# Kernel tuning notes

Measured on AMD Instinct MI355X. Metric: run time of the kernel, lower is better.

## Reference

```python
import jax, jax.numpy as jnp
import numpy as np

HSP, WSP = 8, 32
HEADS = 6
EPS = 1e-5


def _ln(x, g, b):
    m = x.mean(-1, keepdims=True)
    v = ((x - m) ** 2).mean(-1, keepdims=True)
    return (x - m) / jnp.sqrt(v + EPS) * g + b


def _pos_mlp(rpe, pw0, pb0, g1, be1, w1, b1, g2, be2, w2, b2, g3, be3, w3, b3):
    # DynamicPosBias (residual=False): pos3(pos2(pos1(pos_proj(biases))))
    x = rpe @ pw0.T + pb0
    x = jax.nn.relu(_ln(x, g1, be1)) @ w1.T + b1
    x = jax.nn.relu(_ln(x, g2, be2)) @ w2.T + b2
    x = jax.nn.relu(_ln(x, g3, be3)) @ w3.T + b3
    return x  # (n_bias, HEADS)


def setup_inputs() -> dict:
    key = jax.random.key(0)
    ks = jax.random.split(key, 8)
    B, H, W, C = 4, 128, 256, 192
    L = H * W
    pd = (C // 4) // 4  # pos_dim = 12
    nbias = (2 * HSP - 1) * (2 * WSP - 1)  # 945
    N = HSP * WSP  # 256
    nW = L // N  # 128
    f32 = jnp.float32
    return {
        "qkv": jax.random.normal(ks[0], (3, B, L, C), f32),
        "mask": jax.random.normal(ks[1], (nW, N, N), f32),
        "rpe_biases": jax.random.normal(ks[2], (nbias, 2), f32),
        "pw0": jax.random.normal(ks[3], (pd, 2), f32) * 0.02,
        "pb0": jnp.zeros((pd,), f32),
        "g1": jnp.ones((pd,), f32),
        "be1": jnp.zeros((pd,), f32),
        "w1": jax.random.normal(ks[4], (pd, pd), f32) * 0.02,
        "b1": jnp.zeros((pd,), f32),
        "g2": jnp.ones((pd,), f32),
        "be2": jnp.zeros((pd,), f32),
        "w2": jax.random.normal(ks[5], (pd, pd), f32) * 0.02,
        "b2": jnp.zeros((pd,), f32),
        "g3": jnp.ones((pd,), f32),
        "be3": jnp.zeros((pd,), f32),
        "w3": jax.random.normal(ks[6], (HEADS, pd), f32) * 0.02,
        "b3": jnp.zeros((HEADS,), f32),
        "rpi": jax.random.randint(ks[7], (N, N), 0, nbias),
        "H": H,
        "W": W,
    }


def reference(qkv, mask, rpe_biases, pw0, pb0, g1, be1, w1, b1, g2, be2, w2, b2, g3, be3, w3, b3, rpi, H, W):
    _, B, L, C = qkv.shape
    hd = C // HEADS
    scale = hd ** -0.5
    N = HSP * WSP

    def im2win(x):  # (B,L,C) -> (B*nW, HEADS, N, hd)
        x = x.reshape(B, H // HSP, HSP, W // WSP, WSP, C)
        x = x.transpose(0, 1, 3, 2, 4, 5).reshape(-1, N, HEADS, hd)
        return x.transpose(0, 2, 1, 3)

    q = im2win(qkv[0]) * scale
    k = im2win(qkv[1])
    v = im2win(qkv[2])
    attn = jnp.einsum('whnd,whmd->whnm', q, k)  # (B*nW, HEADS, N, N)
    pos = _pos_mlp(rpe_biases, pw0, pb0, g1, be1, w1, b1, g2, be2, w2, b2, g3, be3, w3, b3)
    rpb = pos[rpi.reshape(-1)].reshape(N, N, HEADS).transpose(2, 0, 1)  # (HEADS,N,N)
    attn = attn + rpb[None]
    nW = mask.shape[0]
    attn = attn.reshape(B, nW, HEADS, N, N) + mask[None, :, None]
    attn = jax.nn.softmax(attn, axis=-1).reshape(-1, HEADS, N, N)
    x = (attn @ v).transpose(0, 2, 1, 3).reshape(-1, N, C)  # (B*nW, N, C)
    # windows2img
    x = x.reshape(B, H // HSP, W // WSP, HSP, WSP, C).transpose(0, 1, 3, 2, 4, 5).reshape(B, H, W, C)
    return x
```

## Files before the change

### kernel.cpp

```cpp
#include <hip/hip_runtime.h>

#define EPS 1e-5f
#define LOG2E 1.4426950408889634f
#define QSCALE (0.17677669529663687f * 1.4426950408889634f)

typedef __attribute__((ext_vector_type(8))) short bf16x8;
typedef __attribute__((ext_vector_type(4))) float f32x4;

#if __has_builtin(__builtin_amdgcn_exp2f)
#define EXP2F(x) __builtin_amdgcn_exp2f(x)
#else
#define EXP2F(x) exp2f(x)
#endif

__device__ __forceinline__ unsigned short f2bf(float f) {
  unsigned u = __float_as_uint(f);
  return (unsigned short)((u + 0x7FFFu + ((u >> 16) & 1u)) >> 16);
}
__device__ __forceinline__ float bflo(unsigned u) { return __uint_as_float(u << 16); }
__device__ __forceinline__ float bfhi(unsigned u) { return __uint_as_float(u & 0xFFFF0000u); }

__global__ void pos_mlp_kernel(const float* __restrict__ rpe,
                               const float* __restrict__ pw0, const float* __restrict__ pb0,
                               const float* __restrict__ g1, const float* __restrict__ be1,
                               const float* __restrict__ w1, const float* __restrict__ b1,
                               const float* __restrict__ g2, const float* __restrict__ be2,
                               const float* __restrict__ w2, const float* __restrict__ b2,
                               const float* __restrict__ g3, const float* __restrict__ be3,
                               const float* __restrict__ w3, const float* __restrict__ b3,
                               float* __restrict__ posT) {
  int r = blockIdx.x * blockDim.x + threadIdx.x;
  if (r >= 945) return;
  float a = rpe[2 * r], c = rpe[2 * r + 1];
  float x[12], y[12];
#pragma unroll
  for (int i = 0; i < 12; ++i) x[i] = pw0[2 * i] * a + pw0[2 * i + 1] * c + pb0[i];

  auto stage = [&](const float* g, const float* be, const float* w, const float* bb,
                   const float* in, float* outv, int dout) {
    float m = 0.f;
#pragma unroll
    for (int i = 0; i < 12; ++i) m += in[i];
    m *= (1.f / 12.f);
    float v = 0.f;
#pragma unroll
    for (int i = 0; i < 12; ++i) { float d = in[i] - m; v += d * d; }
    v *= (1.f / 12.f);
    float rs = rsqrtf(v + EPS);
    float t[12];
#pragma unroll
    for (int i = 0; i < 12; ++i) t[i] = fmaxf((in[i] - m) * rs * g[i] + be[i], 0.f);
    for (int o = 0; o < dout; ++o) {
      float s = bb[o];
#pragma unroll
      for (int i = 0; i < 12; ++i) s += w[o * 12 + i] * t[i];
      outv[o] = s;
    }
  };
  stage(g1, be1, w1, b1, x, y, 12);
  stage(g2, be2, w2, b2, y, x, 12);
  stage(g3, be3, w3, b3, x, y, 6);
#pragma unroll
  for (int h = 0; h < 6; ++h) posT[h * 945 + r] = y[h];
}

__global__ void rpb_gather_swz(const int* __restrict__ rpi, const float* __restrict__ posT,
                               unsigned short* __restrict__ rpb) {
  int n2 = blockIdx.x * 256 + threadIdx.x;
  int q = n2 >> 8, key = n2 & 255;
  int idx = rpi[n2];
  int s = ((key >> 5) << 13) + (q << 5) + (key & 31);
#pragma unroll
  for (int h = 0; h < 6; ++h) rpb[(h << 16) + s] = f2bf(posT[h * 945 + idx] * LOG2E);
}

__global__ void mask_cvt_swz(const float* __restrict__ src, uint4* __restrict__ dst) {
  int g = blockIdx.x * 256 + threadIdx.x;
  int wimg = g >> 13;
  int rem = g & 8191;
  int q = rem >> 5;
  int k8 = rem & 31;
  const float* m = src + ((size_t)wimg << 16) + (q << 8) + (k8 << 3);
  float4 a0 = *(const float4*)m;
  float4 a1 = *(const float4*)(m + 4);
  unsigned v0 = (unsigned)f2bf(a0.x * LOG2E) | ((unsigned)f2bf(a0.y * LOG2E) << 16);
  unsigned v1 = (unsigned)f2bf(a0.z * LOG2E) | ((unsigned)f2bf(a0.w * LOG2E) << 16);
  unsigned v2 = (unsigned)f2bf(a1.x * LOG2E) | ((unsigned)f2bf(a1.y * LOG2E) << 16);
  unsigned v3 = (unsigned)f2bf(a1.z * LOG2E) | ((unsigned)f2bf(a1.w * LOG2E) << 16);
  uint4 o; o.x = v0; o.y = v1; o.z = v2; o.w = v3;
  dst[(((size_t)wimg << 16) + ((k8 >> 2) << 13) + (q << 5) + ((k8 & 3) << 3)) >> 3] = o;
}

template <int USEBF>
__global__ __launch_bounds__(512, 6) void attn_kernel(
    const float* __restrict__ qkv, const float* __restrict__ maskf,
    const unsigned short* __restrict__ maskb, const unsigned short* __restrict__ rpb,
    float* __restrict__ out) {
  __shared__ unsigned short Kb[10240];
  __shared__ unsigned short Vt[8448];

  const int tid = threadIdx.x;
  const int wv = tid >> 6;
  const int lane = tid & 63;
  const int quad = lane >> 4;
  const int l16 = lane & 15;
  const int wIdx = blockIdx.x, h = blockIdx.y;
  const int b = wIdx >> 7, wimg = wIdx & 127;
  const int wh = wimg >> 3, ww = wimg & 7;

  {
    const int tok = tid >> 3;
    const int c4 = (tid & 7) << 2;
#pragma unroll
    for (int p = 0; p < 4; ++p) {
      int n = (p << 6) + tok;
      int i = n >> 5, j = n & 31;
      int l = ((wh << 3) + i) * 256 + (ww << 5) + j;
      const float* kp = qkv + ((size_t)((4 + b) * 32768 + l)) * 192 + h * 32 + c4;
      const float* vp = qkv + ((size_t)((8 + b) * 32768 + l)) * 192 + h * 32 + c4;
      float4 kk = *(const float4*)kp;
      float4 vvv = *(const float4*)vp;
      unsigned long long pk = (unsigned long long)f2bf(kk.x) |
                              ((unsigned long long)f2bf(kk.y) << 16) |
                              ((unsigned long long)f2bf(kk.z) << 32) |
                              ((unsigned long long)f2bf(kk.w) << 48);
      int c = n & 31;
      int rowp = (n & ~31) | ((c & 4) << 2) | ((c & 24) >> 1) | (c & 3);
      *(unsigned long long*)(&Kb[rowp * 40 + c4]) = pk;
      Vt[(c4 + 0) * 264 + n] = f2bf(vvv.x);
      Vt[(c4 + 1) * 264 + n] = f2bf(vvv.y);
      Vt[(c4 + 2) * 264 + n] = f2bf(vvv.z);
      Vt[(c4 + 3) * 264 + n] = f2bf(vvv.w);
    }
  }

  bf16x8 qf[2];
#pragma unroll
  for (int rt = 0; rt < 2; ++rt) {
    int n = (wv << 5) + (rt << 4) + l16;
    int i = n >> 5, j = n & 31;
    int l = ((wh << 3) + i) * 256 + (ww << 5) + j;
    const float* qp = qkv + ((size_t)(b * 32768 + l)) * 192 + h * 32 + (quad << 3);
    float4 a0 = *(const float4*)qp;
    float4 a1 = *(const float4*)(qp + 4);
    bf16x8 f;
    f[0] = (short)f2bf(a0.x * QSCALE); f[1] = (short)f2bf(a0.y * QSCALE);
    f[2] = (short)f2bf(a0.z * QSCALE); f[3] = (short)f2bf(a0.w * QSCALE);
    f[4] = (short)f2bf(a1.x * QSCALE); f[5] = (short)f2bf(a1.y * QSCALE);
    f[6] = (short)f2bf(a1.z * QSCALE); f[7] = (short)f2bf(a1.w * QSCALE);
    qf[rt] = f;
  }

  __syncthreads();

  f32x4 Oacc[2][2];
#pragma unroll
  for (int rt = 0; rt < 2; ++rt) {
    Oacc[rt][0] = (f32x4){0.f, 0.f, 0.f, 0.f};
    Oacc[rt][1] = (f32x4){0.f, 0.f, 0.f, 0.f};
  }
  float lsum[2] = {0.f, 0.f};

  const unsigned short* rp = rpb + ((size_t)h << 16);
  const unsigned short* mp = maskb + ((size_t)wimg << 16);
  const float* mfp0 = maskf + ((size_t)wimg << 16);
  const int boff = (((wv << 5) + l16) << 5) + (quad << 3);
  const f32x4 zero = (f32x4){0.f, 0.f, 0.f, 0.f};

  for (int cc = 0; cc < 8; ++cc) {
    const int cb = cc << 5;
    const int tof = cc << 13;
    uint4 pr[2], mr[2];
#pragma unroll
    for (int rt = 0; rt < 2; ++rt) {
      int o0 = tof + boff + (rt << 9);
      pr[rt] = *(const uint4*)(rp + o0);
      if (USEBF) mr[rt] = *(const uint4*)(mp + o0);
    }
    bf16x8 kf0 = *(const bf16x8*)(&Kb[(cb + l16) * 40 + (quad << 3)]);
    bf16x8 kf1 = *(const bf16x8*)(&Kb[(cb + 16 + l16) * 40 + (quad << 3)]);
    bf16x8 vf0 = *(const bf16x8*)(&Vt[l16 * 264 + cb + (quad << 3)]);
    bf16x8 vf1 = *(const bf16x8*)(&Vt[(16 + l16) * 264 + cb + (quad << 3)]);
#pragma unroll
    for (int rt = 0; rt < 2; ++rt) {
      __builtin_amdgcn_s_setprio(1);
      f32x4 S0 = __builtin_amdgcn_mfma_f32_16x16x32_bf16(kf0, qf[rt], zero, 0, 0, 0);
      f32x4 S1 = __builtin_amdgcn_mfma_f32_16x16x32_bf16(kf1, qf[rt], zero, 0, 0, 0);
      __builtin_amdgcn_s_setprio(0);
      float m_[8], p_[8];
      if (USEBF) {
        m_[0] = bflo(mr[rt].x); m_[1] = bfhi(mr[rt].x);
        m_[2] = bflo(mr[rt].y); m_[3] = bfhi(mr[rt].y);
        m_[4] = bflo(mr[rt].z); m_[5] = bfhi(mr[rt].z);
        m_[6] = bflo(mr[rt].w); m_[7] = bfhi(mr[rt].w);
      } else {
        int qrow = (wv << 5) + (rt << 4) + l16;
        float4 f0 = *(const float4*)(mfp0 + (qrow << 8) + cb + (quad << 3));
        float4 f1 = *(const float4*)(mfp0 + (qrow << 8) + cb + (quad << 3) + 4);
        m_[0] = f0.x * LOG2E; m_[1] = f0.y * LOG2E; m_[2] = f0.z * LOG2E; m_[3] = f0.w * LOG2E;
        m_[4] = f1.x * LOG2E; m_[5] = f1.y * LOG2E; m_[6] = f1.z * LOG2E; m_[7] = f1.w * LOG2E;
      }
      p_[0] = bflo(pr[rt].x); p_[1] = bfhi(pr[rt].x);
      p_[2] = bflo(pr[rt].y); p_[3] = bfhi(pr[rt].y);
      p_[4] = bflo(pr[rt].z); p_[5] = bfhi(pr[rt].z);
      p_[6] = bflo(pr[rt].w); p_[7] = bfhi(pr[rt].w);
      float e[8];
#pragma unroll
      for (int r = 0; r < 4; ++r) {
        e[r]     = EXP2F(S0[r] + m_[r] + p_[r]);
        e[4 + r] = EXP2F(S1[r] + m_[4 + r] + p_[4 + r]);
      }
      lsum[rt] += ((e[0] + e[1]) + (e[2] + e[3])) + ((e[4] + e[5]) + (e[6] + e[7]));
      union PF { unsigned w[4]; bf16x8 v; } u;
      u.w[0] = (unsigned)f2bf(e[0]) | ((unsigned)f2bf(e[1]) << 16);
      u.w[1] = (unsigned)f2bf(e[2]) | ((unsigned)f2bf(e[3]) << 16);
      u.w[2] = (unsigned)f2bf(e[4]) | ((unsigned)f2bf(e[5]) << 16);
      u.w[3] = (unsigned)f2bf(e[6]) | ((unsigned)f2bf(e[7]) << 16);
      __builtin_amdgcn_s_setprio(1);
      Oacc[rt][0] = __builtin_amdgcn_mfma_f32_16x16x32_bf16(u.v, vf0, Oacc[rt][0], 0, 0, 0);
      Oacc[rt][1] = __builtin_amdgcn_mfma_f32_16x16x32_bf16(u.v, vf1, Oacc[rt][1], 0, 0, 0);
      __builtin_amdgcn_s_setprio(0);
    }
  }

#pragma unroll
  for (int rt = 0; rt < 2; ++rt) {
    float v = lsum[rt];
    v += __shfl_xor(v, 16);
    v += __shfl_xor(v, 32);
    float inv = 1.0f / v;
    int n0 = (wv << 5) + (rt << 4) + (quad << 2);
#pragma unroll
    for (int r = 0; r < 4; ++r) {
      float ir = __shfl(inv, (quad << 4) + (quad << 2) + r);
      int n = n0 + r;
      int i = n >> 5, j = n & 31;
      size_t o = ((size_t)((b * 128 + (wh << 3) + i) * 256 + (ww << 5) + j)) * 192 + h * 32 + l16;
      out[o] = Oacc[rt][0][r] * ir;
      out[o + 16] = Oacc[rt][1][r] * ir;
    }
  }
}

extern "C" void kernel_launch(void* const* d_in, const int* in_sizes, int n_in,
                              void* d_out, int out_size, void* d_ws, size_t ws_size,
                              hipStream_t stream) {
  const float* qkv = (const float*)d_in[0];
  const float* mask = (const float*)d_in[1];
  const float* rpe = (const float*)d_in[2];
  const float* pw0 = (const float*)d_in[3];
  const float* pb0 = (const float*)d_in[4];
  const float* g1 = (const float*)d_in[5];
  const float* be1 = (const float*)d_in[6];
  const float* w1 = (const float*)d_in[7];
  const float* b1 = (const float*)d_in[8];
  const float* g2 = (const float*)d_in[9];
  const float* be2 = (const float*)d_in[10];
  const float* w2 = (const float*)d_in[11];
  const float* b2 = (const float*)d_in[12];
  const float* g3 = (const float*)d_in[13];
  const float* be3 = (const float*)d_in[14];
  const float* w3 = (const float*)d_in[15];
  const float* b3 = (const float*)d_in[16];
  const int* rpi = (const int*)d_in[17];
  float* out = (float*)d_out;

  char* ws = (char*)d_ws;
  float* posT = (float*)ws;
  unsigned short* rpb = (unsigned short*)(ws + 22784);
  unsigned short* mb = (unsigned short*)(ws + 22784 + 786432);
  const size_t need_mb = 22784 + 786432 + 16777216;
  const int use_bf = (ws_size >= need_mb) ? 1 : 0;

  pos_mlp_kernel<<<4, 256, 0, stream>>>(rpe, pw0, pb0, g1, be1, w1, b1, g2, be2, w2, b2,
                                        g3, be3, w3, b3, posT);
  rpb_gather_swz<<<256, 256, 0, stream>>>(rpi, posT, rpb);
  if (use_bf)
    mask_cvt_swz<<<4096, 256, 0, stream>>>(mask, (uint4*)mb);

  dim3 grid(512, 6);
  if (use_bf)
    attn_kernel<1><<<grid, 512, 0, stream>>>(qkv, mask, mb, rpb, out);
  else
    attn_kernel<0><<<grid, 512, 0, stream>>>(qkv, mask, mb, rpb, out);
}
```

Measured before the change: 568.4 us.

## Software-pipeline bias/mask and K/V fragment loads across attention chunks

Restructures the chunk loop into a two-stage ping-pong: rpb/mask global loads and K/V LDS fragment reads for the next chunk are issued before computing the current one, and the first bias load is hoisted above the barrier. This is meant to hide global and LDS latency behind the MFMA/exp work. The extra prefetch registers led to lowering the launch-bounds occupancy hint from 6 to 4 blocks per CU, which trades fewer resident waves for more registers. The last iteration does a redundant wrap-around prefetch of chunk 0.

```diff
diff --git a/kernel.cpp b/kernel.cpp
--- a/kernel.cpp
+++ b/kernel.cpp
@@ -92,7 +92,7 @@
 }
 
 template <int USEBF>
-__global__ __launch_bounds__(512, 6) void attn_kernel(
+__global__ __launch_bounds__(512, 4) void attn_kernel(
     const float* __restrict__ qkv, const float* __restrict__ maskf,
     const unsigned short* __restrict__ maskb, const unsigned short* __restrict__ rpb,
     float* __restrict__ out) {
@@ -151,48 +151,49 @@
     qf[rt] = f;
   }
 
-  __syncthreads();
-
-  f32x4 Oacc[2][2];
-#pragma unroll
-  for (int rt = 0; rt < 2; ++rt) {
-    Oacc[rt][0] = (f32x4){0.f, 0.f, 0.f, 0.f};
-    Oacc[rt][1] = (f32x4){0.f, 0.f, 0.f, 0.f};
-  }
-  float lsum[2] = {0.f, 0.f};
-
   const unsigned short* rp = rpb + ((size_t)h << 16);
   const unsigned short* mp = maskb + ((size_t)wimg << 16);
   const float* mfp0 = maskf + ((size_t)wimg << 16);
   const int boff = (((wv << 5) + l16) << 5) + (quad << 3);
   const f32x4 zero = (f32x4){0.f, 0.f, 0.f, 0.f};
 
-  for (int cc = 0; cc < 8; ++cc) {
-    const int cb = cc << 5;
-    const int tof = cc << 13;
-    uint4 pr[2], mr[2];
+  f32x4 Oacc[2][2];
+#pragma unroll
+  for (int rt = 0; rt < 2; ++rt) {
+    Oacc[rt][0] = (f32x4){0.f, 0.f, 0.f, 0.f};
+    Oacc[rt][1] = (f32x4){0.f, 0.f, 0.f, 0.f};
+  }
+  float lsum[2] = {0.f, 0.f};
+
+  auto pf_bias = [&](int c, uint4* prq, uint4* mrq) {
 #pragma unroll
     for (int rt = 0; rt < 2; ++rt) {
-      int o0 = tof + boff + (rt << 9);
-      pr[rt] = *(const uint4*)(rp + o0);
-      if (USEBF) mr[rt] = *(const uint4*)(mp + o0);
-    }
-    bf16x8 kf0 = *(const bf16x8*)(&Kb[(cb + l16) * 40 + (quad << 3)]);
-    bf16x8 kf1 = *(const bf16x8*)(&Kb[(cb + 16 + l16) * 40 + (quad << 3)]);
-    bf16x8 vf0 = *(const bf16x8*)(&Vt[l16 * 264 + cb + (quad << 3)]);
-    bf16x8 vf1 = *(const bf16x8*)(&Vt[(16 + l16) * 264 + cb + (quad << 3)]);
+      int o0 = (c << 13) + boff + (rt << 9);
+      prq[rt] = *(const uint4*)(rp + o0);
+      if (USEBF) mrq[rt] = *(const uint4*)(mp + o0);
+    }
+  };
+  auto pf_kv = [&](int c, bf16x8* kf, bf16x8* vf) {
+    int cbn = c << 5;
+    kf[0] = *(const bf16x8*)(&Kb[(cbn + l16) * 40 + (quad << 3)]);
+    kf[1] = *(const bf16x8*)(&Kb[(cbn + 16 + l16) * 40 + (quad << 3)]);
+    vf[0] = *(const bf16x8*)(&Vt[l16 * 264 + cbn + (quad << 3)]);
+    vf[1] = *(const bf16x8*)(&Vt[(16 + l16) * 264 + cbn + (quad << 3)]);
+  };
+  auto body = [&](int cb, const uint4* prq, const uint4* mrq,
+                  const bf16x8* kf, const bf16x8* vf) {
 #pragma unroll
     for (int rt = 0; rt < 2; ++rt) {
       __builtin_amdgcn_s_setprio(1);
-      f32x4 S0 = __builtin_amdgcn_mfma_f32_16x16x32_bf16(kf0, qf[rt], zero, 0, 0, 0);
-      f32x4 S1 = __builtin_amdgcn_mfma_f32_16x16x32_bf16(kf1, qf[rt], zero, 0, 0, 0);
+      f32x4 S0 = __builtin_amdgcn_mfma_f32_16x16x32_bf16(kf[0], qf[rt], zero, 0, 0, 0);
+      f32x4 S1 = __builtin_amdgcn_mfma_f32_16x16x32_bf16(kf[1], qf[rt], zero, 0, 0, 0);
       __builtin_amdgcn_s_setprio(0);
       float m_[8], p_[8];
       if (USEBF) {
-        m_[0] = bflo(mr[rt].x); m_[1] = bfhi(mr[rt].x);
-        m_[2] = bflo(mr[rt].y); m_[3] = bfhi(mr[rt].y);
-        m_[4] = bflo(mr[rt].z); m_[5] = bfhi(mr[rt].z);
-        m_[6] = bflo(mr[rt].w); m_[7] = bfhi(mr[rt].w);
+        m_[0] = bflo(mrq[rt].x); m_[1] = bfhi(mrq[rt].x);
+        m_[2] = bflo(mrq[rt].y); m_[3] = bfhi(mrq[rt].y);
+        m_[4] = bflo(mrq[rt].z); m_[5] = bfhi(mrq[rt].z);
+        m_[6] = bflo(mrq[rt].w); m_[7] = bfhi(mrq[rt].w);
       } else {
         int qrow = (wv << 5) + (rt << 4) + l16;
         float4 f0 = *(const float4*)(mfp0 + (qrow << 8) + cb + (quad << 3));
@@ -200,10 +201,10 @@
         m_[0] = f0.x * LOG2E; m_[1] = f0.y * LOG2E; m_[2] = f0.z * LOG2E; m_[3] = f0.w * LOG2E;
         m_[4] = f1.x * LOG2E; m_[5] = f1.y * LOG2E; m_[6] = f1.z * LOG2E; m_[7] = f1.w * LOG2E;
       }
-      p_[0] = bflo(pr[rt].x); p_[1] = bfhi(pr[rt].x);
-      p_[2] = bflo(pr[rt].y); p_[3] = bfhi(pr[rt].y);
-      p_[4] = bflo(pr[rt].z); p_[5] = bfhi(pr[rt].z);
-      p_[6] = bflo(pr[rt].w); p_[7] = bfhi(pr[rt].w);
+      p_[0] = bflo(prq[rt].x); p_[1] = bfhi(prq[rt].x);
+      p_[2] = bflo(prq[rt].y); p_[3] = bfhi(prq[rt].y);
+      p_[4] = bflo(prq[rt].z); p_[5] = bfhi(prq[rt].z);
+      p_[6] = bflo(prq[rt].w); p_[7] = bfhi(prq[rt].w);
       float e[8];
 #pragma unroll
       for (int r = 0; r < 4; ++r) {
@@ -217,10 +218,28 @@
       u.w[2] = (unsigned)f2bf(e[4]) | ((unsigned)f2bf(e[5]) << 16);
       u.w[3] = (unsigned)f2bf(e[6]) | ((unsigned)f2bf(e[7]) << 16);
       __builtin_amdgcn_s_setprio(1);
-      Oacc[rt][0] = __builtin_amdgcn_mfma_f32_16x16x32_bf16(u.v, vf0, Oacc[rt][0], 0, 0, 0);
-      Oacc[rt][1] = __builtin_amdgcn_mfma_f32_16x16x32_bf16(u.v, vf1, Oacc[rt][1], 0, 0, 0);
+      Oacc[rt][0] = __builtin_amdgcn_mfma_f32_16x16x32_bf16(u.v, vf[0], Oacc[rt][0], 0, 0, 0);
+      Oacc[rt][1] = __builtin_amdgcn_mfma_f32_16x16x32_bf16(u.v, vf[1], Oacc[rt][1], 0, 0, 0);
       __builtin_amdgcn_s_setprio(0);
     }
+  };
+
+  uint4 prA[2], mrA[2], prB[2], mrB[2];
+  bf16x8 kfA[2], vfA[2], kfB[2], vfB[2];
+  pf_bias(0, prA, mrA);
+
+  __syncthreads();
+
+  pf_kv(0, kfA, vfA);
+
+#pragma unroll 1
+  for (int cc = 0; cc < 8; cc += 2) {
+    pf_bias(cc + 1, prB, mrB);
+    pf_kv(cc + 1, kfB, vfB);
+    body(cc << 5, prA, mrA, kfA, vfA);
+    pf_bias((cc + 2) & 7, prA, mrA);
+    pf_kv((cc + 2) & 7, kfA, vfA);
+    body((cc + 1) << 5, prB, mrB, kfB, vfB);
   }
 
 #pragma unroll
```

New measurement: 599.1 us. 1.05x slower.
